# Performance work log

Hardware: AMD Instinct MI355X
Metric: run time of the kernel (lower is better)

## Reference

```python
import jax, jax.numpy as jnp
import numpy as np

D = 512; L = 8; NH = 8; BS = 32; HW = 32; VA = 8; HA = 8; SEQ = 2 * VA * HA
DK = D // NH  # per-head dim
LN_EPS = 1e-5


def setup_inputs() -> dict:
    key = jax.random.key(0)
    ks = iter(jax.random.split(key, 40))
    def rn(shape, s=0.02):
        return (s * jax.random.normal(next(ks), shape)).astype(jnp.float32)
    inp = {
        'rgb_fea': jax.random.normal(next(ks), (BS, D, HW, HW), jnp.float32),
        'ir_fea':  jax.random.normal(next(ks), (BS, D, HW, HW), jnp.float32),
        'pos_emb': rn((1, SEQ, D)),
        'conv1_w': rn((8, D), 0.05),    # 1x1 conv, stored [out,in]
        'conv2_w': rn((D, 8), 0.05),
        'ln1_w': jnp.ones((L, D)), 'ln1_b': jnp.zeros((L, D)),
        'Wq': rn((L, D, D)), 'bq': jnp.zeros((L, D)),
        'Wk': rn((L, D, D)), 'bk': jnp.zeros((L, D)),
        'Wv': rn((L, D, D)), 'bv': jnp.zeros((L, D)),
        'Wo': rn((L, D, D)), 'bo': jnp.zeros((L, D)),
        'ln2_w': jnp.ones((L, D)), 'ln2_b': jnp.zeros((L, D)),
        'W1': rn((L, D, 4 * D)), 'b1': jnp.zeros((L, 4 * D)),
        'W2': rn((L, 4 * D, D)), 'b2': jnp.zeros((L, D)),
        'lnf_w': jnp.ones((D,)), 'lnf_b': jnp.zeros((D,)),
    }
    return inp


def _ln(x, w, b):
    m = x.mean(-1, keepdims=True)
    v = jnp.var(x, axis=-1, keepdims=True)
    return (x - m) / jnp.sqrt(v + LN_EPS) * w + b


def _avgpool8(x):
    b, c, h, w = x.shape
    return x.reshape(b, c, VA, h // VA, HA, w // HA).mean(axis=(3, 5))


def _highpass(x):
    # extract_frequency2: fftshifted FFT, zero the [crow-thr:crow+thr, ccol-thr:ccol+thr]
    # block (Python slice semantics, negative start wraps), then inverse FFT.
    rows, cols = x.shape[-2], x.shape[-1]
    crow, ccol = rows // 2, cols // 2
    thr = crow + ccol // 4
    f = jnp.fft.fftshift(jnp.fft.fftn(x, axes=(-2, -1)), axes=(-2, -1))
    f = f.at[:, :, crow - thr:crow + thr, ccol - thr:ccol + thr].set(0)
    hp = jnp.fft.ifftn(jnp.fft.ifftshift(f, axes=(-2, -1)), axes=(-2, -1))
    return hp.real  # real part (torch code casts to half; real part is the runnable interpretation)


def _block(x, p):
    ln1 = _ln(x, p['ln1_w'], p['ln1_b'])
    q = (ln1 @ p['Wq'] + p['bq']).reshape(BS, SEQ, NH, DK).transpose(0, 2, 1, 3)
    k = (ln1 @ p['Wk'] + p['bk']).reshape(BS, SEQ, NH, DK).transpose(0, 2, 1, 3)
    v = (ln1 @ p['Wv'] + p['bv']).reshape(BS, SEQ, NH, DK).transpose(0, 2, 1, 3)
    att = jax.nn.softmax(jnp.einsum('bhqd,bhkd->bhqk', q, k) / np.sqrt(DK), axis=-1)
    o = jnp.einsum('bhqk,bhkd->bhqd', att, v).transpose(0, 2, 1, 3).reshape(BS, SEQ, D)
    x = x + o @ p['Wo'] + p['bo']
    ln2 = _ln(x, p['ln2_w'], p['ln2_b'])
    h = jax.nn.gelu(ln2 @ p['W1'] + p['b1'], approximate=False)
    x = x + h @ p['W2'] + p['b2']
    return x, None


def reference(rgb_fea, ir_fea, pos_emb, conv1_w, conv2_w, ln1_w, ln1_b,
              Wq, bq, Wk, bk, Wv, bv, Wo, bo, ln2_w, ln2_b,
              W1, b1, W2, b2, lnf_w, lnf_b):
    bs, c, h, w = rgb_fea.shape
    rgb_p = _avgpool8(rgb_fea)
    ir_p = _avgpool8(ir_fea)
    rgb_hp = _highpass(rgb_p)
    ir_hp = _highpass(ir_p)

    conv1 = lambda t: jnp.einsum('bchw,oc->bohw', t, conv1_w)
    rgb_hp_M = jax.nn.sigmoid(conv1(rgb_hp * rgb_p))
    ir_hp_M = jax.nn.sigmoid(conv1(ir_hp * ir_p))
    rgb_M = jax.nn.sigmoid(conv1(rgb_p))
    ir_M = jax.nn.sigmoid(conv1(ir_p))

    hw = VA * HA
    half = (bs * 8) // 8  # = bs
    M = jnp.concatenate([rgb_M.reshape(-1, hw), ir_M.reshape(-1, hw),
                         rgb_hp_M.reshape(-1, hw)[:half], ir_hp_M.reshape(-1, hw)[:half]], axis=0)
    l = M.shape[0]
    s = M.sum(0)
    # sum_{i<j} M_i . M_j = (||sum_i M_i||^2 - sum_i ||M_i||^2) / 2
    patten_loss = (jnp.dot(s, s) - jnp.sum(M * M)) * 0.5 / (l * (l - 1))

    P_rgb = jnp.einsum('bchw,oc->bohw', rgb_M, conv2_w) * rgb_p
    P_ir = jnp.einsum('bchw,oc->bohw', ir_M, conv2_w) * ir_p

    tok = jnp.concatenate([P_rgb.reshape(bs, c, -1), P_ir.reshape(bs, c, -1)], axis=2)
    x = pos_emb + tok.transpose(0, 2, 1)  # [bs, 2*VA*HA, d]

    layer = {'ln1_w': ln1_w, 'ln1_b': ln1_b, 'Wq': Wq, 'bq': bq, 'Wk': Wk, 'bk': bk,
             'Wv': Wv, 'bv': bv, 'Wo': Wo, 'bo': bo, 'ln2_w': ln2_w, 'ln2_b': ln2_b,
             'W1': W1, 'b1': b1, 'W2': W2, 'b2': b2}
    x, _ = jax.lax.scan(_block, x, layer)
    x = _ln(x, lnf_w, lnf_b)

    x = x.reshape(bs, 2, VA, HA, D).transpose(0, 1, 4, 2, 3)  # [bs,2,d,VA,HA]
    rgb_out = jax.image.resize(x[:, 0], (bs, D, h, w), method='bilinear')
    ir_out = jax.image.resize(x[:, 1], (bs, D, h, w), method='bilinear')
    return rgb_out, ir_out, patten_loss
```

## Files before the change

### kernel.cpp

```cpp
#include <hip/hip_runtime.h>
#include <math.h>

typedef unsigned short u16;
typedef short v8s __attribute__((ext_vector_type(8)));
typedef float v4f __attribute__((ext_vector_type(4)));

#define MTOT 4096

__device__ __forceinline__ u16 f2bf(float f) {
  unsigned int u = __float_as_uint(f);
  u += 0x7fffu + ((u >> 16) & 1u);
  return (u16)(u >> 16);
}

__device__ __forceinline__ v4f mfma16(v8s a, v8s b, v4f c) {
  return __builtin_amdgcn_mfma_f32_16x16x32_bf16(a, b, c, 0, 0, 0);
}

__device__ __forceinline__ void gl_lds16(const u16* g, u16* l) {
  __builtin_amdgcn_global_load_lds(
      (const __attribute__((address_space(1))) void*)g,
      (__attribute__((address_space(3))) void*)l, 16, 0, 0);
}

__constant__ float c_ct[8] = {1.f, -0.70710678118654752f, 0.f, 0.70710678118654752f,
                              -1.f, 0.70710678118654752f, 0.f, -0.70710678118654752f};
__constant__ float c_st[8] = {0.f, 0.70710678118654752f, -1.f, 0.70710678118654752f,
                              0.f, -0.70710678118654752f, 1.f, -0.70710678118654752f};

__global__ __launch_bounds__(256) void transpose_bf16_kernel(
    const float* __restrict__ src, u16* __restrict__ dst,
    int K, int N, size_t srcLS, size_t dstLS, int rowOff)
{
  int l = blockIdx.z;
  int n0 = blockIdx.x * 32, k0 = blockIdx.y * 32;
  __shared__ float tile[32][33];
  int tx = threadIdx.x & 31, ty = threadIdx.x >> 5;
  const float* s = src + (size_t)l * srcLS;
#pragma unroll
  for (int rr = 0; rr < 4; ++rr) {
    int k = k0 + ty + rr * 8;
    tile[ty + rr * 8][tx] = s[(size_t)k * N + n0 + tx];
  }
  __syncthreads();
  u16* dp = dst + (size_t)l * dstLS;
#pragma unroll
  for (int rr = 0; rr < 4; ++rr) {
    int n = n0 + ty + rr * 8;
    dp[(size_t)(rowOff + n) * K + k0 + tx] = f2bf(tile[tx][ty + rr * 8]);
  }
}

__global__ __launch_bounds__(256) void qkvbias_kernel(
    const float* __restrict__ bq, const float* __restrict__ bk,
    const float* __restrict__ bv, float* __restrict__ qb)
{
  int l = blockIdx.x;
  for (int j = threadIdx.x; j < 1536; j += 256) {
    float v = (j < 512) ? bq[l * 512 + j] : (j < 1024) ? bk[l * 512 + j - 512] : bv[l * 512 + j - 1024];
    qb[l * 1536 + j] = v;
  }
}

__global__ __launch_bounds__(256) void pool_kernel(
    const float* __restrict__ rgb, const float* __restrict__ ir, float* __restrict__ pool)
{
  int idx = blockIdx.x * 4 + (threadIdx.x >> 6);
  int i = threadIdx.x & 63;
  int y = i >> 3, xcol = i & 7;
  int timg = idx >> 14;
  int rem = idx & 16383;
  const float* src = (timg ? ir : rgb) + (size_t)rem * 1024;
  float s = 0.f;
#pragma unroll
  for (int r = 0; r < 4; ++r) {
    float4 v = *(const float4*)(src + (y * 4 + r) * 32 + xcol * 4);
    s += v.x + v.y + v.z + v.w;
  }
  pool[(size_t)idx * 64 + i] = s * 0.0625f;
}

__global__ __launch_bounds__(256) void convm_kernel(
    const float* __restrict__ pool, const float* __restrict__ conv1_w,
    float* __restrict__ Mplain, float* __restrict__ Mhp)
{
  int bid = blockIdx.x;
  int kind, timg, b;
  if (bid < 64) { kind = 0; timg = bid >> 5; b = bid & 31; }
  else { int y = bid - 64; kind = 1; timg = y >> 2; b = y & 3; }
  int t = threadIdx.x, hw = t & 63, cg = t >> 6;
  int yy = hw >> 3, xx = hw & 7;
  int sd = (yy + xx) & 7;
  float ct = c_ct[sd], st = c_st[sd];
  float acc[8] = {0.f,0.f,0.f,0.f,0.f,0.f,0.f,0.f};
  const float* pbase = pool + ((size_t)(timg * 32 + b) * 512) * 64;
  for (int c = cg; c < 512; c += 4) {
    float p = pbase[c * 64 + hw];
    float val = p;
    if (kind == 1) {
      float C = p * ct, S = p * st;
#pragma unroll
      for (int d = 1; d < 64; d <<= 1) { C += __shfl_xor(C, d, 64); S += __shfl_xor(S, d, 64); }
      float hp = p - (C * ct + S * st) * (1.0f / 64.0f);
      val = hp * p;
    }
#pragma unroll
    for (int o = 0; o < 8; ++o) acc[o] += conv1_w[o * 512 + c] * val;
  }
  __shared__ float red[4][8][64];
#pragma unroll
  for (int o = 0; o < 8; ++o) red[cg][o][hw] = acc[o];
  __syncthreads();
  if (cg == 0) {
#pragma unroll
    for (int o = 0; o < 8; ++o) {
      float s = red[0][o][hw] + red[1][o][hw] + red[2][o][hw] + red[3][o][hw];
      float m = 1.0f / (1.0f + expf(-s));
      if (kind == 0) Mplain[((size_t)(timg * 32 + b) * 8 + o) * 64 + hw] = m;
      else           Mhp[((size_t)(timg * 4 + b) * 8 + o) * 64 + hw] = m;
    }
  }
}

__global__ __launch_bounds__(256) void loss_kernel(
    const float* __restrict__ Mplain, const float* __restrict__ Mhp, float* __restrict__ out)
{
  int t = threadIdx.x, col = t & 63, rg = t >> 6;
  float sp = 0.f, sq = 0.f;
  for (int r = rg; r < 576; r += 4) {
    const float* rowp = (r < 512) ? (Mplain + (size_t)r * 64) : (Mhp + (size_t)(r - 512) * 64);
    float v = rowp[col];
    sp += v; sq += v * v;
  }
  __shared__ float scol[4][64], ssq[4][64];
  scol[rg][col] = sp; ssq[rg][col] = sq;
  __syncthreads();
  if (t < 64) {
    float s = scol[0][t] + scol[1][t] + scol[2][t] + scol[3][t];
    float q = ssq[0][t] + ssq[1][t] + ssq[2][t] + ssq[3][t];
    float ds = s * s;
#pragma unroll
    for (int d = 1; d < 64; d <<= 1) { ds += __shfl_xor(ds, d, 64); q += __shfl_xor(q, d, 64); }
    if (t == 0) *out = (ds - q) * 0.5f / (576.0f * 575.0f);
  }
}

__global__ __launch_bounds__(256) void token_kernel(
    const float* __restrict__ pos_emb, const float* __restrict__ conv2_w,
    const float* __restrict__ Mplain, const float* __restrict__ pool, float* __restrict__ x)
{
  int bs_idx = blockIdx.x;
  int b = bs_idx >> 7, s = bs_idx & 127;
  int timg = s >> 6, hw = s & 63;
  __shared__ float Ms[8];
  if (threadIdx.x < 8)
    Ms[threadIdx.x] = Mplain[((size_t)(timg * 32 + b) * 8 + threadIdx.x) * 64 + hw];
  __syncthreads();
#pragma unroll
  for (int i = 0; i < 2; ++i) {
    int d = threadIdx.x + i * 256;
    float acc = 0.f;
#pragma unroll
    for (int o = 0; o < 8; ++o) acc += conv2_w[d * 8 + o] * Ms[o];
    float p = pool[(((size_t)timg * 32 + b) * 512 + d) * 64 + hw];
    x[(size_t)bs_idx * 512 + d] = pos_emb[s * 512 + d] + acc * p;
  }
}

template<int OBF>
__global__ __launch_bounds__(256) void ln_kernel(
    const float* __restrict__ xin, const float* __restrict__ w,
    const float* __restrict__ bb, void* __restrict__ out)
{
  int row = blockIdx.x, t = threadIdx.x;
  float2 v = ((const float2*)(xin + (size_t)row * 512))[t];
  float s = v.x + v.y, q = v.x * v.x + v.y * v.y;
#pragma unroll
  for (int d = 1; d < 64; d <<= 1) { s += __shfl_xor(s, d, 64); q += __shfl_xor(q, d, 64); }
  __shared__ float ps[4], pq[4];
  int wv = t >> 6;
  if ((t & 63) == 0) { ps[wv] = s; pq[wv] = q; }
  __syncthreads();
  float S = ps[0] + ps[1] + ps[2] + ps[3];
  float Q = pq[0] + pq[1] + pq[2] + pq[3];
  float mean = S * (1.0f / 512.0f);
  float var = Q * (1.0f / 512.0f) - mean * mean;
  float rstd = rsqrtf(var + 1e-5f);
  float o0 = (v.x - mean) * rstd * w[t * 2] + bb[t * 2];
  float o1 = (v.y - mean) * rstd * w[t * 2 + 1] + bb[t * 2 + 1];
  if (OBF) { u16* o = (u16*)out + (size_t)row * 512; o[t * 2] = f2bf(o0); o[t * 2 + 1] = f2bf(o1); }
  else     { float* o = (float*)out + (size_t)row * 512; o[t * 2] = o0; o[t * 2 + 1] = o1; }
}

template<int ACT, int RESID, int OBF>
__global__ __launch_bounds__(256) void gemm_bt(
    const u16* __restrict__ A, const u16* __restrict__ BT,
    const float* __restrict__ bias, const float* __restrict__ resid,
    void* __restrict__ Cout, int N, int K)
{
  __shared__ u16 As[128 * 32];
  __shared__ u16 Bs[128 * 32];
  const int m0 = blockIdx.y * 128, n0 = blockIdx.x * 128;
  const int t = threadIdx.x, lane = t & 63, w = t >> 6;
  const int lr = lane & 15, lq = lane >> 4;
  const int wm = (w & 1) * 64, wn = (w >> 1) * 64;
  v4f acc[4][4];
  const v4f vzero = {0.f, 0.f, 0.f, 0.f};
#pragma unroll
  for (int mt = 0; mt < 4; ++mt)
#pragma unroll
    for (int nt = 0; nt < 4; ++nt) acc[mt][nt] = vzero;

  for (int kk = 0; kk < K; kk += 32) {
    __syncthreads();
    {
      int r0 = t >> 2, c0 = (t & 3) << 3;
      gl_lds16(A  + (size_t)(m0 + r0) * K + kk + c0, As + (size_t)(w * 64) * 8);
      gl_lds16(BT + (size_t)(n0 + r0) * K + kk + c0, Bs + (size_t)(w * 64) * 8);
      int ch = 256 + t;
      int r1 = ch >> 2, c1 = (ch & 3) << 3;
      gl_lds16(A  + (size_t)(m0 + r1) * K + kk + c1, As + (size_t)(256 + w * 64) * 8);
      gl_lds16(BT + (size_t)(n0 + r1) * K + kk + c1, Bs + (size_t)(256 + w * 64) * 8);
    }
    __syncthreads();
    v8s a[4], b[4];
#pragma unroll
    for (int mt = 0; mt < 4; ++mt)
      a[mt] = *(const v8s*)(As + (wm + mt * 16 + lr) * 32 + lq * 8);
#pragma unroll
    for (int nt = 0; nt < 4; ++nt)
      b[nt] = *(const v8s*)(Bs + (wn + nt * 16 + lr) * 32 + lq * 8);
#pragma unroll
    for (int mt = 0; mt < 4; ++mt)
#pragma unroll
      for (int nt = 0; nt < 4; ++nt)
        acc[mt][nt] = mfma16(a[mt], b[nt], acc[mt][nt]);
  }

#pragma unroll
  for (int mt = 0; mt < 4; ++mt)
#pragma unroll
    for (int nt = 0; nt < 4; ++nt) {
      int col = n0 + wn + nt * 16 + lr;
      float bsv = bias[col];
#pragma unroll
      for (int r = 0; r < 4; ++r) {
        int row = m0 + wm + mt * 16 + lq * 4 + r;
        float v = acc[mt][nt][r] + bsv;
        if (ACT == 1) v = 0.5f * v * (1.0f + erff(v * 0.70710678118654752f));
        if (RESID) v += resid[(size_t)row * N + col];
        if (OBF) ((u16*)Cout)[(size_t)row * N + col] = f2bf(v);
        else     ((float*)Cout)[(size_t)row * N + col] = v;
      }
    }
}

__global__ __launch_bounds__(256) void attn_kernel(
    const u16* __restrict__ qkv, u16* __restrict__ attn_out)
{
  __shared__ u16 Ks[128 * 64];
  __shared__ u16 Vt[64 * 128];
  __shared__ u16 Ps[128 * 128];
  const int h = blockIdx.x, b = blockIdx.y;
  const int t = threadIdx.x, lane = t & 63, w = t >> 6;
  const int lr = lane & 15, lq = lane >> 4;
  const u16* base = qkv + (size_t)b * 128 * 1536 + h * 64;

#pragma unroll
  for (int i = 0; i < 4; ++i) {
    int ch = i * 256 + t;
    int s = ch >> 3, off = (ch & 7) * 8;
    *(v8s*)(Ks + s * 64 + off) = *(const v8s*)(base + 512 + (size_t)s * 1536 + off);
    v8s vv = *(const v8s*)(base + 1024 + (size_t)s * 1536 + off);
#pragma unroll
    for (int j = 0; j < 8; ++j) Vt[(off + j) * 128 + s] = (u16)vv[j];
  }
  __syncthreads();

  const v4f vzero = {0.f, 0.f, 0.f, 0.f};
  v4f sacc[2][8];
#pragma unroll
  for (int mt = 0; mt < 2; ++mt)
#pragma unroll
    for (int nt = 0; nt < 8; ++nt) sacc[mt][nt] = vzero;
#pragma unroll
  for (int kk = 0; kk < 64; kk += 32) {
    v8s a0 = *(const v8s*)(base + (size_t)(w * 32 + lr) * 1536 + kk + lq * 8);
    v8s a1 = *(const v8s*)(base + (size_t)(w * 32 + 16 + lr) * 1536 + kk + lq * 8);
#pragma unroll
    for (int nt = 0; nt < 8; ++nt) {
      v8s bb = *(const v8s*)(Ks + (nt * 16 + lr) * 64 + kk + lq * 8);
      sacc[0][nt] = mfma16(a0, bb, sacc[0][nt]);
      sacc[1][nt] = mfma16(a1, bb, sacc[1][nt]);
    }
  }

  float rinv[2][4];
#pragma unroll
  for (int mt = 0; mt < 2; ++mt)
#pragma unroll
    for (int r = 0; r < 4; ++r) {
      float mx = -3.0e38f;
#pragma unroll
      for (int nt = 0; nt < 8; ++nt) mx = fmaxf(mx, sacc[mt][nt][r]);
#pragma unroll
      for (int d = 1; d < 16; d <<= 1) mx = fmaxf(mx, __shfl_xor(mx, d, 64));
      float ls = 0.f;
      float pv[8];
#pragma unroll
      for (int nt = 0; nt < 8; ++nt) {
        pv[nt] = expf((sacc[mt][nt][r] - mx) * 0.125f);
        ls += pv[nt];
      }
#pragma unroll
      for (int d = 1; d < 16; d <<= 1) ls += __shfl_xor(ls, d, 64);
      rinv[mt][r] = 1.0f / ls;
      int row = w * 32 + mt * 16 + lq * 4 + r;
#pragma unroll
      for (int nt = 0; nt < 8; ++nt) Ps[row * 128 + nt * 16 + lr] = f2bf(pv[nt]);
    }
  __syncthreads();

  v4f oacc[2][4];
#pragma unroll
  for (int mt = 0; mt < 2; ++mt)
#pragma unroll
    for (int nt = 0; nt < 4; ++nt) oacc[mt][nt] = vzero;
#pragma unroll
  for (int kk = 0; kk < 128; kk += 32) {
    v8s a0 = *(const v8s*)(Ps + (w * 32 + lr) * 128 + kk + lq * 8);
    v8s a1 = *(const v8s*)(Ps + (w * 32 + 16 + lr) * 128 + kk + lq * 8);
#pragma unroll
    for (int nt = 0; nt < 4; ++nt) {
      v8s bb = *(const v8s*)(Vt + (nt * 16 + lr) * 128 + kk + lq * 8);
      oacc[0][nt] = mfma16(a0, bb, oacc[0][nt]);
      oacc[1][nt] = mfma16(a1, bb, oacc[1][nt]);
    }
  }
#pragma unroll
  for (int mt = 0; mt < 2; ++mt)
#pragma unroll
    for (int nt = 0; nt < 4; ++nt)
#pragma unroll
      for (int r = 0; r < 4; ++r) {
        int row = w * 32 + mt * 16 + lq * 4 + r;
        int col = nt * 16 + lr;
        attn_out[((size_t)(b * 128 + row)) * 512 + h * 64 + col] =
            f2bf(oacc[mt][nt][r] * rinv[mt][r]);
      }
}

__global__ __launch_bounds__(256) void upsample_kernel(
    const float* __restrict__ xf, float* __restrict__ out)
{
  int bid = blockIdx.x;
  int c = bid & 511;
  int tb = bid >> 9;
  int b = tb & 31, timg = tb >> 5;
  __shared__ float tile[64];
  if (threadIdx.x < 64) {
    int s = timg * 64 + threadIdx.x;
    tile[threadIdx.x] = xf[((size_t)b * 128 + s) * 512 + c];
  }
  __syncthreads();
  float* obase = out + (size_t)timg * (32ull * 512 * 1024) + ((size_t)b * 512 + c) * 1024;
#pragma unroll
  for (int k = 0; k < 4; ++k) {
    int pix = threadIdx.x + k * 256;
    int i = pix >> 5, j = pix & 31;
    float cy = fminf(fmaxf((i - 1.5f) * 0.25f, 0.f), 7.f);
    float cx = fminf(fmaxf((j - 1.5f) * 0.25f, 0.f), 7.f);
    int y0 = (int)cy, x0 = (int)cx;
    int y1 = min(y0 + 1, 7), x1 = min(x0 + 1, 7);
    float fy = cy - y0, fx = cx - x0;
    float v00 = tile[y0 * 8 + x0], v01 = tile[y0 * 8 + x1];
    float v10 = tile[y1 * 8 + x0], v11 = tile[y1 * 8 + x1];
    obase[pix] = (v00 * (1.f - fx) + v01 * fx) * (1.f - fy) + (v10 * (1.f - fx) + v11 * fx) * fy;
  }
}

extern "C" void kernel_launch(void* const* d_in, const int* in_sizes, int n_in,
                              void* d_out, int out_size, void* d_ws, size_t ws_size,
                              hipStream_t stream)
{
  const float* rgb_fea = (const float*)d_in[0];
  const float* ir_fea  = (const float*)d_in[1];
  const float* pos_emb = (const float*)d_in[2];
  const float* conv1_w = (const float*)d_in[3];
  const float* conv2_w = (const float*)d_in[4];
  const float* ln1_w = (const float*)d_in[5];
  const float* ln1_b = (const float*)d_in[6];
  const float* Wq = (const float*)d_in[7];
  const float* bq = (const float*)d_in[8];
  const float* Wk = (const float*)d_in[9];
  const float* bk = (const float*)d_in[10];
  const float* Wv = (const float*)d_in[11];
  const float* bv = (const float*)d_in[12];
  const float* Wo = (const float*)d_in[13];
  const float* bo = (const float*)d_in[14];
  const float* ln2_w = (const float*)d_in[15];
  const float* ln2_b = (const float*)d_in[16];
  const float* W1 = (const float*)d_in[17];
  const float* b1 = (const float*)d_in[18];
  const float* W2 = (const float*)d_in[19];
  const float* b2 = (const float*)d_in[20];
  const float* lnf_w = (const float*)d_in[21];
  const float* lnf_b = (const float*)d_in[22];
  (void)in_sizes; (void)n_in; (void)out_size; (void)ws_size;

  char* wsb = (char*)d_ws;
  size_t off = 0;
  auto alloc = [&](size_t nbytes) -> void* {
    void* p = wsb + off;
    off += (nbytes + 255) & ~(size_t)255;
    return p;
  };
  float* pool   = (float*)alloc(2ull * 32 * 512 * 64 * 4);
  float* Mplain = (float*)alloc(2ull * 32 * 8 * 64 * 4);
  float* Mhp    = (float*)alloc(2ull * 4 * 8 * 64 * 4);
  float* x      = (float*)alloc((size_t)MTOT * 512 * 4);
  float* xf     = (float*)alloc((size_t)MTOT * 512 * 4);
  u16* ln_out   = (u16*)alloc((size_t)MTOT * 512 * 2);
  u16* qkv      = (u16*)alloc((size_t)MTOT * 1536 * 2);
  u16* attn     = (u16*)alloc((size_t)MTOT * 512 * 2);
  u16* hbuf     = (u16*)alloc((size_t)MTOT * 2048 * 2);
  u16* WqkvT    = (u16*)alloc(8ull * 1536 * 512 * 2);
  u16* WoT      = (u16*)alloc(8ull * 512 * 512 * 2);
  u16* W1T      = (u16*)alloc(8ull * 2048 * 512 * 2);
  u16* W2T      = (u16*)alloc(8ull * 512 * 2048 * 2);
  float* qb     = (float*)alloc(8ull * 1536 * 4);

  transpose_bf16_kernel<<<dim3(16, 16, 8), 256, 0, stream>>>(Wq, WqkvT, 512, 512, 512ull * 512, 1536ull * 512, 0);
  transpose_bf16_kernel<<<dim3(16, 16, 8), 256, 0, stream>>>(Wk, WqkvT, 512, 512, 512ull * 512, 1536ull * 512, 512);
  transpose_bf16_kernel<<<dim3(16, 16, 8), 256, 0, stream>>>(Wv, WqkvT, 512, 512, 512ull * 512, 1536ull * 512, 1024);
  transpose_bf16_kernel<<<dim3(16, 16, 8), 256, 0, stream>>>(Wo, WoT, 512, 512, 512ull * 512, 512ull * 512, 0);
  transpose_bf16_kernel<<<dim3(64, 16, 8), 256, 0, stream>>>(W1, W1T, 512, 2048, 512ull * 2048, 2048ull * 512, 0);
  transpose_bf16_kernel<<<dim3(16, 64, 8), 256, 0, stream>>>(W2, W2T, 2048, 512, 2048ull * 512, 512ull * 2048, 0);
  qkvbias_kernel<<<8, 256, 0, stream>>>(bq, bk, bv, qb);

  pool_kernel<<<8192, 256, 0, stream>>>(rgb_fea, ir_fea, pool);
  convm_kernel<<<72, 256, 0, stream>>>(pool, conv1_w, Mplain, Mhp);
  loss_kernel<<<1, 256, 0, stream>>>(Mplain, Mhp, (float*)d_out + 33554432);
  token_kernel<<<MTOT, 256, 0, stream>>>(pos_emb, conv2_w, Mplain, pool, x);

  for (int l = 0; l < 8; ++l) {
    ln_kernel<1><<<MTOT, 256, 0, stream>>>(x, ln1_w + l * 512, ln1_b + l * 512, ln_out);
    gemm_bt<0, 0, 1><<<dim3(12, 32), 256, 0, stream>>>(
        ln_out, WqkvT + (size_t)l * 1536 * 512, qb + l * 1536, nullptr, qkv, 1536, 512);
    attn_kernel<<<dim3(8, 32), 256, 0, stream>>>(qkv, attn);
    gemm_bt<0, 1, 0><<<dim3(4, 32), 256, 0, stream>>>(
        attn, WoT + (size_t)l * 512 * 512, bo + l * 512, x, x, 512, 512);
    ln_kernel<1><<<MTOT, 256, 0, stream>>>(x, ln2_w + l * 512, ln2_b + l * 512, ln_out);
    gemm_bt<1, 0, 1><<<dim3(16, 32), 256, 0, stream>>>(
        ln_out, W1T + (size_t)l * 2048 * 512, b1 + l * 2048, nullptr, hbuf, 2048, 512);
    gemm_bt<0, 1, 0><<<dim3(4, 32), 256, 0, stream>>>(
        hbuf, W2T + (size_t)l * 512 * 2048, b2 + l * 512, x, x, 512, 2048);
  }

  ln_kernel<0><<<MTOT, 256, 0, stream>>>(x, lnf_w, lnf_b, xf);
  upsample_kernel<<<32768, 256, 0, stream>>>(xf, (float*)d_out);
}
```

Measured before the change: 1.517 ms.

## Split channel reduction in convm, use 128x64 GEMM tiles for N=512 GEMMs

The convm kernel is split across 8 channel chunks, grid 72x8 instead of 72 blocks. Partial sums go to a scratch buffer, and a new msig kernel reduces them and applies the sigmoid. The two N=512 GEMMs (attention output projection and FFN down-projection) move to a new 128x64 tile kernel, which doubles the block count from 128 to 256 to fill more CUs. The three Q/K/V weight transposes are merged into one launch. The costs are an extra kernel launch and scratch traffic for convm, and less operand reuse per block in the smaller-tile GEMM.

```diff
diff --git a/kernel.cpp b/kernel.cpp
--- a/kernel.cpp
+++ b/kernel.cpp
@@ -48,6 +48,32 @@
   for (int rr = 0; rr < 4; ++rr) {
     int n = n0 + ty + rr * 8;
     dp[(size_t)(rowOff + n) * K + k0 + tx] = f2bf(tile[tx][ty + rr * 8]);
+  }
+}
+
+__global__ __launch_bounds__(256) void qkv_transpose_kernel(
+    const float* __restrict__ Wq, const float* __restrict__ Wk,
+    const float* __restrict__ Wv, u16* __restrict__ dst)
+{
+  int z = blockIdx.z;
+  int l = z / 3, which = z % 3;
+  const float* src = (which == 0) ? Wq : (which == 1) ? Wk : Wv;
+  int n0 = blockIdx.x * 32, k0 = blockIdx.y * 32;
+  __shared__ float tile[32][33];
+  int tx = threadIdx.x & 31, ty = threadIdx.x >> 5;
+  const float* s = src + (size_t)l * 512 * 512;
+#pragma unroll
+  for (int rr = 0; rr < 4; ++rr) {
+    int k = k0 + ty + rr * 8;
+    tile[ty + rr * 8][tx] = s[(size_t)k * 512 + n0 + tx];
+  }
+  __syncthreads();
+  u16* dp = dst + (size_t)l * 1536 * 512;
+  int rowOff = which * 512;
+#pragma unroll
+  for (int rr = 0; rr < 4; ++rr) {
+    int n = n0 + ty + rr * 8;
+    dp[(size_t)(rowOff + n) * 512 + k0 + tx] = f2bf(tile[tx][ty + rr * 8]);
   }
 }
 
@@ -82,20 +108,25 @@
 
 __global__ __launch_bounds__(256) void convm_kernel(
     const float* __restrict__ pool, const float* __restrict__ conv1_w,
-    float* __restrict__ Mplain, float* __restrict__ Mhp)
-{
-  int bid = blockIdx.x;
-  int kind, timg, b;
-  if (bid < 64) { kind = 0; timg = bid >> 5; b = bid & 31; }
-  else { int y = bid - 64; kind = 1; timg = y >> 2; b = y & 3; }
+    float* __restrict__ Macc)
+{
+  int r = blockIdx.x;
+  int cc = blockIdx.y;
   int t = threadIdx.x, hw = t & 63, cg = t >> 6;
+  int kind = (r < 64) ? 0 : 1;
+  int prow;
+  if (kind == 0) prow = r;
+  else { int rh = r - 64; prow = (rh >> 2) * 32 + (rh & 3); }
   int yy = hw >> 3, xx = hw & 7;
   int sd = (yy + xx) & 7;
   float ct = c_ct[sd], st = c_st[sd];
   float acc[8] = {0.f,0.f,0.f,0.f,0.f,0.f,0.f,0.f};
-  const float* pbase = pool + ((size_t)(timg * 32 + b) * 512) * 64;
-  for (int c = cg; c < 512; c += 4) {
-    float p = pbase[c * 64 + hw];
+  const float* pbase = pool + ((size_t)prow * 512 + cc * 64) * 64;
+#pragma unroll 4
+  for (int it = 0; it < 16; ++it) {
+    int cl = cg * 16 + it;
+    int c = cc * 64 + cl;
+    float p = pbase[(size_t)cl * 64 + hw];
     float val = p;
     if (kind == 1) {
       float C = p * ct, S = p * st;
@@ -115,11 +146,21 @@
 #pragma unroll
     for (int o = 0; o < 8; ++o) {
       float s = red[0][o][hw] + red[1][o][hw] + red[2][o][hw] + red[3][o][hw];
-      float m = 1.0f / (1.0f + expf(-s));
-      if (kind == 0) Mplain[((size_t)(timg * 32 + b) * 8 + o) * 64 + hw] = m;
-      else           Mhp[((size_t)(timg * 4 + b) * 8 + o) * 64 + hw] = m;
-    }
-  }
+      Macc[((size_t)cc * 72 + r) * 512 + o * 64 + hw] = s;
+    }
+  }
+}
+
+__global__ __launch_bounds__(256) void msig_kernel(
+    const float* __restrict__ Macc, float* __restrict__ Mplain, float* __restrict__ Mhp)
+{
+  int i = blockIdx.x * 256 + threadIdx.x;
+  float s = 0.f;
+#pragma unroll
+  for (int cc = 0; cc < 8; ++cc) s += Macc[(size_t)cc * 72 * 512 + i];
+  float m = 1.0f / (1.0f + expf(-s));
+  if (i < 64 * 512) Mplain[i] = m;
+  else Mhp[i - 64 * 512] = m;
 }
 
 __global__ __launch_bounds__(256) void loss_kernel(
@@ -241,6 +282,68 @@
   for (int mt = 0; mt < 4; ++mt)
 #pragma unroll
     for (int nt = 0; nt < 4; ++nt) {
+      int col = n0 + wn + nt * 16 + lr;
+      float bsv = bias[col];
+#pragma unroll
+      for (int r = 0; r < 4; ++r) {
+        int row = m0 + wm + mt * 16 + lq * 4 + r;
+        float v = acc[mt][nt][r] + bsv;
+        if (ACT == 1) v = 0.5f * v * (1.0f + erff(v * 0.70710678118654752f));
+        if (RESID) v += resid[(size_t)row * N + col];
+        if (OBF) ((u16*)Cout)[(size_t)row * N + col] = f2bf(v);
+        else     ((float*)Cout)[(size_t)row * N + col] = v;
+      }
+    }
+}
+
+template<int ACT, int RESID, int OBF>
+__global__ __launch_bounds__(256) void gemm_bt64(
+    const u16* __restrict__ A, const u16* __restrict__ BT,
+    const float* __restrict__ bias, const float* __restrict__ resid,
+    void* __restrict__ Cout, int N, int K)
+{
+  __shared__ u16 As[128 * 32];
+  __shared__ u16 Bs[64 * 32];
+  const int m0 = blockIdx.y * 128, n0 = blockIdx.x * 64;
+  const int t = threadIdx.x, lane = t & 63, w = t >> 6;
+  const int lr = lane & 15, lq = lane >> 4;
+  const int wm = (w & 1) * 64, wn = (w >> 1) * 32;
+  v4f acc[4][2];
+  const v4f vzero = {0.f, 0.f, 0.f, 0.f};
+#pragma unroll
+  for (int mt = 0; mt < 4; ++mt)
+#pragma unroll
+    for (int nt = 0; nt < 2; ++nt) acc[mt][nt] = vzero;
+
+  for (int kk = 0; kk < K; kk += 32) {
+    __syncthreads();
+    {
+      int r0 = t >> 2, c0 = (t & 3) << 3;
+      gl_lds16(A  + (size_t)(m0 + r0) * K + kk + c0, As + (size_t)(w * 64) * 8);
+      gl_lds16(BT + (size_t)(n0 + r0) * K + kk + c0, Bs + (size_t)(w * 64) * 8);
+      int ch = 256 + t;
+      int r1 = ch >> 2, c1 = (ch & 3) << 3;
+      gl_lds16(A  + (size_t)(m0 + r1) * K + kk + c1, As + (size_t)(256 + w * 64) * 8);
+    }
+    __syncthreads();
+    v8s a[4], b[2];
+#pragma unroll
+    for (int mt = 0; mt < 4; ++mt)
+      a[mt] = *(const v8s*)(As + (wm + mt * 16 + lr) * 32 + lq * 8);
+#pragma unroll
+    for (int nt = 0; nt < 2; ++nt)
+      b[nt] = *(const v8s*)(Bs + (wn + nt * 16 + lr) * 32 + lq * 8);
+#pragma unroll
+    for (int mt = 0; mt < 4; ++mt)
+#pragma unroll
+      for (int nt = 0; nt < 2; ++nt)
+        acc[mt][nt] = mfma16(a[mt], b[nt], acc[mt][nt]);
+  }
+
+#pragma unroll
+  for (int mt = 0; mt < 4; ++mt)
+#pragma unroll
+    for (int nt = 0; nt < 2; ++nt) {
       int col = n0 + wn + nt * 16 + lr;
       float bsv = bias[col];
 #pragma unroll
@@ -416,6 +519,7 @@
     return p;
   };
   float* pool   = (float*)alloc(2ull * 32 * 512 * 64 * 4);
+  float* Macc   = (float*)alloc(8ull * 72 * 512 * 4);
   float* Mplain = (float*)alloc(2ull * 32 * 8 * 64 * 4);
   float* Mhp    = (float*)alloc(2ull * 4 * 8 * 64 * 4);
   float* x      = (float*)alloc((size_t)MTOT * 512 * 4);
@@ -430,16 +534,15 @@
   u16* W2T      = (u16*)alloc(8ull * 512 * 2048 * 2);
   float* qb     = (float*)alloc(8ull * 1536 * 4);
 
-  transpose_bf16_kernel<<<dim3(16, 16, 8), 256, 0, stream>>>(Wq, WqkvT, 512, 512, 512ull * 512, 1536ull * 512, 0);
-  transpose_bf16_kernel<<<dim3(16, 16, 8), 256, 0, stream>>>(Wk, WqkvT, 512, 512, 512ull * 512, 1536ull * 512, 512);
-  transpose_bf16_kernel<<<dim3(16, 16, 8), 256, 0, stream>>>(Wv, WqkvT, 512, 512, 512ull * 512, 1536ull * 512, 1024);
+  qkv_transpose_kernel<<<dim3(16, 16, 24), 256, 0, stream>>>(Wq, Wk, Wv, WqkvT);
   transpose_bf16_kernel<<<dim3(16, 16, 8), 256, 0, stream>>>(Wo, WoT, 512, 512, 512ull * 512, 512ull * 512, 0);
   transpose_bf16_kernel<<<dim3(64, 16, 8), 256, 0, stream>>>(W1, W1T, 512, 2048, 512ull * 2048, 2048ull * 512, 0);
   transpose_bf16_kernel<<<dim3(16, 64, 8), 256, 0, stream>>>(W2, W2T, 2048, 512, 2048ull * 512, 512ull * 2048, 0);
   qkvbias_kernel<<<8, 256, 0, stream>>>(bq, bk, bv, qb);
 
   pool_kernel<<<8192, 256, 0, stream>>>(rgb_fea, ir_fea, pool);
-  convm_kernel<<<72, 256, 0, stream>>>(pool, conv1_w, Mplain, Mhp);
+  convm_kernel<<<dim3(72, 8), 256, 0, stream>>>(pool, conv1_w, Macc);
+  msig_kernel<<<144, 256, 0, stream>>>(Macc, Mplain, Mhp);
   loss_kernel<<<1, 256, 0, stream>>>(Mplain, Mhp, (float*)d_out + 33554432);
   token_kernel<<<MTOT, 256, 0, stream>>>(pos_emb, conv2_w, Mplain, pool, x);
 
@@ -448,12 +551,12 @@
     gemm_bt<0, 0, 1><<<dim3(12, 32), 256, 0, stream>>>(
         ln_out, WqkvT + (size_t)l * 1536 * 512, qb + l * 1536, nullptr, qkv, 1536, 512);
     attn_kernel<<<dim3(8, 32), 256, 0, stream>>>(qkv, attn);
-    gemm_bt<0, 1, 0><<<dim3(4, 32), 256, 0, stream>>>(
+    gemm_bt64<0, 1, 0><<<dim3(8, 32), 256, 0, stream>>>(
         attn, WoT + (size_t)l * 512 * 512, bo + l * 512, x, x, 512, 512);
     ln_kernel<1><<<MTOT, 256, 0, stream>>>(x, ln2_w + l * 512, ln2_b + l * 512, ln_out);
     gemm_bt<1, 0, 1><<<dim3(16, 32), 256, 0, stream>>>(
         ln_out, W1T + (size_t)l * 2048 * 512, b1 + l * 2048, nullptr, hbuf, 2048, 512);
-    gemm_bt<0, 1, 0><<<dim3(4, 32), 256, 0, stream>>>(
+    gemm_bt64<0, 1, 0><<<dim3(8, 32), 256, 0, stream>>>(
         hbuf, W2T + (size_t)l * 512 * 2048, b2 + l * 512, x, x, 512, 2048);
   }
 
```

New measurement: 1.374 ms. 1.1x faster.
